# Performance work log

Hardware: AMD Instinct MI355X
Metric: run time of the kernel (lower is better)

The kernel has to match this reference:

```python
import jax, jax.numpy as jnp
import numpy as np

NUM_TYPES = 4
SPLINE_GRID = 5   # grid centers on [0, 1]
SPLINE_SPAN = 3   # number of overlapping basis functions -> degree P = 2
CHANNELS = 64
E = 500_000
P = SPLINE_SPAN - 1
NUM_BASIS = (SPLINE_GRID - 1) + P  # intervals + degree = 6


def _knots_np():
    # uniform knots extended by P beyond each end of [0, 1]
    h = 1.0 / (SPLINE_GRID - 1)
    return ((np.arange(NUM_BASIS + P + 1) - P) * h).astype(np.float32)


def bspline_basis(x):
    """Uniform B-spline basis of degree P via Cox-de Boor. x: [E] in [0,1] -> [E, NUM_BASIS]."""
    t = jnp.asarray(_knots_np(), dtype=x.dtype)
    xe = jnp.clip(x, 0.0, 1.0 - 1e-6)[:, None]
    # degree-0: indicator of the knot interval  [E, NUM_BASIS + P]
    B = ((xe >= t[None, :-1]) & (xe < t[None, 1:])).astype(x.dtype)
    for k in range(1, P + 1):
        left = (xe - t[None, : -(k + 1)]) / (t[k:-1] - t[: -(k + 1)])[None, :] * B[:, :-1]
        right = (t[None, k + 1 :] - xe) / (t[k + 1 :] - t[1:-k])[None, :] * B[:, 1:]
        B = left + right
    return B  # [E, NUM_BASIS]


def setup_inputs() -> dict:
    key = jax.random.key(0)
    k1, k2, k3 = jax.random.split(key, 3)
    x = jax.random.uniform(k1, (E,), dtype=jnp.float32)                 # normalized edge lengths in [0,1]
    edge_types = jax.random.randint(k2, (2, E), 0, NUM_TYPES)           # (center, neighbor) atom types
    coeffs = jax.random.normal(
        k3, (NUM_TYPES * NUM_TYPES, NUM_BASIS, CHANNELS), dtype=jnp.float32
    )  # per-edge-type spline coefficients
    return {"x": x, "edge_types": edge_types, "coeffs": coeffs}


def reference(x, edge_types, coeffs):
    # edge class = center_type * num_types + neighbor_type
    cls = edge_types[0] * NUM_TYPES + edge_types[1]      # [E]
    basis = bspline_basis(x)                             # [E, NUM_BASIS]
    # gather per-edge coefficients and reduce over the local spline support
    return jnp.einsum("eb,ebc->ec", basis, coeffs[cls])  # [E, CHANNELS]
```

## Files before the change

kernel.cpp:

```cpp
#include <hip/hip_runtime.h>

constexpr int NUM_TYPES    = 4;
constexpr int NUM_BASIS    = 6;
constexpr int CHANNELS     = 64;
constexpr int COEFF_FLOATS = NUM_TYPES * NUM_TYPES * NUM_BASIS * CHANNELS;

typedef float f4 __attribute__((ext_vector_type(4)));
typedef int   i4 __attribute__((ext_vector_type(4)));

__global__ __launch_bounds__(256)
void TwoBodySplineScalarEmbed_kernel(const float* __restrict__ x,
                                     const int*   __restrict__ edge_types,
                                     const float* __restrict__ coeffs,
                                     float*       __restrict__ out,
                                     int E)
{
    __shared__ float sc[COEFF_FLOATS];
    for (int i = threadIdx.x; i < COEFF_FLOATS; i += 256)
        sc[i] = coeffs[i];
    __syncthreads();

    const int laneC = threadIdx.x & 15;
    const int grp   = threadIdx.x >> 4;
    const int c0    = laneC * 4;

    for (int e0 = blockIdx.x * 64 + grp * 4; e0 < E; e0 += gridDim.x * 64)
    {
        if (e0 + 3 < E) {
            f4 xv = *reinterpret_cast<const f4*>(x + e0);
            i4 tc = *reinterpret_cast<const i4*>(edge_types + e0);
            i4 tn = *reinterpret_cast<const i4*>(edge_types + E + e0);

            #pragma unroll
            for (int j = 0; j < 4; ++j) {
                float xj = fminf(fmaxf(xv[j], 0.0f), 1.0f - 1e-6f);
                float s  = xj * 4.0f;
                int   i0 = (int)s;  i0 = i0 > 3 ? 3 : i0;
                float u  = s - (float)i0;
                float omu = 1.0f - u;
                float w0 = 0.5f * omu * omu;
                float w1 = u * omu + 0.5f;
                float w2 = 0.5f * u * u;

                int cls = tc[j] * NUM_TYPES + tn[j];
                const float* base = &sc[(cls * NUM_BASIS + i0) * CHANNELS + c0];
                f4 r0 = *reinterpret_cast<const f4*>(base);
                f4 r1 = *reinterpret_cast<const f4*>(base + CHANNELS);
                f4 r2 = *reinterpret_cast<const f4*>(base + 2 * CHANNELS);

                f4 o = w0 * r0 + w1 * r1 + w2 * r2;
                __builtin_nontemporal_store(
                    o, reinterpret_cast<f4*>(out + (size_t)(e0 + j) * CHANNELS + c0));
            }
        } else {
            for (int j = 0; j < 4; ++j) {
                int e = e0 + j;
                if (e >= E) break;
                float xj = fminf(fmaxf(x[e], 0.0f), 1.0f - 1e-6f);
                float s  = xj * 4.0f;
                int   i0 = (int)s;  i0 = i0 > 3 ? 3 : i0;
                float u  = s - (float)i0;
                float omu = 1.0f - u;
                float w0 = 0.5f * omu * omu;
                float w1 = u * omu + 0.5f;
                float w2 = 0.5f * u * u;

                int cls = edge_types[e] * NUM_TYPES + edge_types[E + e];
                const float* base = &sc[(cls * NUM_BASIS + i0) * CHANNELS + c0];
                f4 r0 = *reinterpret_cast<const f4*>(base);
                f4 r1 = *reinterpret_cast<const f4*>(base + CHANNELS);
                f4 r2 = *reinterpret_cast<const f4*>(base + 2 * CHANNELS);

                f4 o = w0 * r0 + w1 * r1 + w2 * r2;
                __builtin_nontemporal_store(
                    o, reinterpret_cast<f4*>(out + (size_t)e * CHANNELS + c0));
            }
        }
    }
}

extern "C" void kernel_launch(void* const* d_in, const int* in_sizes, int n_in,
                              void* d_out, int out_size, void* d_ws, size_t ws_size,
                              hipStream_t stream)
{
    const float* x          = (const float*)d_in[0];
    const int*   edge_types = (const int*)d_in[1];
    const float* coeffs     = (const float*)d_in[2];
    float*       out        = (float*)d_out;

    const int E = in_sizes[0];

    int grid = (E + 63) / 64;
    if (grid > 1536) grid = 1536;

    TwoBodySplineScalarEmbed_kernel<<<grid, 256, 0, stream>>>(
        x, edge_types, coeffs, out, E);
}
```

Measured before the change: 28.60 us.

## Process one edge per 16-lane group and vectorize coefficient staging

Each 16-lane group now handles a single edge per iteration instead of four, with scalar loads of x and the edge types replacing the vector loads. The coefficient copy into shared memory uses float4 loads, and the output store becomes a regular store instead of a nontemporal one. Together these change the edge-to-thread mapping so consecutive groups write contiguous output rows, removing the tail branch. In exchange it loses per-thread ILP and the cache-bypass hint on the 128 MB output stream, and issues more scalar loads per edge.

```diff
diff --git a/kernel.cpp b/kernel.cpp
--- a/kernel.cpp
+++ b/kernel.cpp
@@ -6,7 +6,6 @@
 constexpr int COEFF_FLOATS = NUM_TYPES * NUM_TYPES * NUM_BASIS * CHANNELS;
 
 typedef float f4 __attribute__((ext_vector_type(4)));
-typedef int   i4 __attribute__((ext_vector_type(4)));
 
 __global__ __launch_bounds__(256)
 void TwoBodySplineScalarEmbed_kernel(const float* __restrict__ x,
@@ -16,66 +15,37 @@
                                      int E)
 {
     __shared__ float sc[COEFF_FLOATS];
-    for (int i = threadIdx.x; i < COEFF_FLOATS; i += 256)
-        sc[i] = coeffs[i];
+    #pragma unroll
+    for (int i = 0; i < COEFF_FLOATS / 4 / 256; ++i) {
+        int idx = threadIdx.x + i * 256;
+        reinterpret_cast<f4*>(sc)[idx] = reinterpret_cast<const f4*>(coeffs)[idx];
+    }
     __syncthreads();
 
-    const int laneC = threadIdx.x & 15;
-    const int grp   = threadIdx.x >> 4;
-    const int c0    = laneC * 4;
+    const int laneC  = threadIdx.x & 15;
+    const int grp    = threadIdx.x >> 4;
+    const int c0     = laneC * 4;
+    const int stride = gridDim.x << 4;
 
-    for (int e0 = blockIdx.x * 64 + grp * 4; e0 < E; e0 += gridDim.x * 64)
+    for (int e = (blockIdx.x << 4) + grp; e < E; e += stride)
     {
-        if (e0 + 3 < E) {
-            f4 xv = *reinterpret_cast<const f4*>(x + e0);
-            i4 tc = *reinterpret_cast<const i4*>(edge_types + e0);
-            i4 tn = *reinterpret_cast<const i4*>(edge_types + E + e0);
+        float xj = fminf(fmaxf(x[e], 0.0f), 1.0f - 1e-6f);
+        float s  = xj * 4.0f;
+        int   i0 = (int)s;  i0 = i0 > 3 ? 3 : i0;
+        float u  = s - (float)i0;
+        float omu = 1.0f - u;
+        float w0 = 0.5f * omu * omu;
+        float w1 = u * omu + 0.5f;
+        float w2 = 0.5f * u * u;
 
-            #pragma unroll
-            for (int j = 0; j < 4; ++j) {
-                float xj = fminf(fmaxf(xv[j], 0.0f), 1.0f - 1e-6f);
-                float s  = xj * 4.0f;
-                int   i0 = (int)s;  i0 = i0 > 3 ? 3 : i0;
-                float u  = s - (float)i0;
-                float omu = 1.0f - u;
-                float w0 = 0.5f * omu * omu;
-                float w1 = u * omu + 0.5f;
-                float w2 = 0.5f * u * u;
+        int row = (edge_types[e] * NUM_TYPES + edge_types[E + e]) * NUM_BASIS + i0;
+        const float* base = &sc[row * CHANNELS + c0];
+        f4 r0 = *reinterpret_cast<const f4*>(base);
+        f4 r1 = *reinterpret_cast<const f4*>(base + CHANNELS);
+        f4 r2 = *reinterpret_cast<const f4*>(base + 2 * CHANNELS);
 
-                int cls = tc[j] * NUM_TYPES + tn[j];
-                const float* base = &sc[(cls * NUM_BASIS + i0) * CHANNELS + c0];
-                f4 r0 = *reinterpret_cast<const f4*>(base);
-                f4 r1 = *reinterpret_cast<const f4*>(base + CHANNELS);
-                f4 r2 = *reinterpret_cast<const f4*>(base + 2 * CHANNELS);
-
-                f4 o = w0 * r0 + w1 * r1 + w2 * r2;
-                __builtin_nontemporal_store(
-                    o, reinterpret_cast<f4*>(out + (size_t)(e0 + j) * CHANNELS + c0));
-            }
-        } else {
-            for (int j = 0; j < 4; ++j) {
-                int e = e0 + j;
-                if (e >= E) break;
-                float xj = fminf(fmaxf(x[e], 0.0f), 1.0f - 1e-6f);
-                float s  = xj * 4.0f;
-                int   i0 = (int)s;  i0 = i0 > 3 ? 3 : i0;
-                float u  = s - (float)i0;
-                float omu = 1.0f - u;
-                float w0 = 0.5f * omu * omu;
-                float w1 = u * omu + 0.5f;
-                float w2 = 0.5f * u * u;
-
-                int cls = edge_types[e] * NUM_TYPES + edge_types[E + e];
-                const float* base = &sc[(cls * NUM_BASIS + i0) * CHANNELS + c0];
-                f4 r0 = *reinterpret_cast<const f4*>(base);
-                f4 r1 = *reinterpret_cast<const f4*>(base + CHANNELS);
-                f4 r2 = *reinterpret_cast<const f4*>(base + 2 * CHANNELS);
-
-                f4 o = w0 * r0 + w1 * r1 + w2 * r2;
-                __builtin_nontemporal_store(
-                    o, reinterpret_cast<f4*>(out + (size_t)e * CHANNELS + c0));
-            }
-        }
+        f4 o = w0 * r0 + w1 * r1 + w2 * r2;
+        *reinterpret_cast<f4*>(out + (size_t)e * CHANNELS + c0) = o;
     }
 }
 
@@ -90,7 +60,7 @@
 
     const int E = in_sizes[0];
 
-    int grid = (E + 63) / 64;
+    int grid = (E + 15) / 16;
     if (grid > 1536) grid = 1536;
 
     TwoBodySplineScalarEmbed_kernel<<<grid, 256, 0, stream>>>(
```

After: 27.74 us. -3.0%, faster.
